# Kernel tuning notes

Hardware: AMD Instinct MI355X
Metric: run time of the kernel (lower is better)

Reference implementation:

```python
import jax, jax.numpy as jnp
import numpy as np

DIM = 1024

def setup_inputs() -> dict:
    key = jax.random.key(0)
    k1, k2, k3, k4 = jax.random.split(key, 4)
    x = jax.random.normal(k1, (4, 2048, DIM), dtype=jnp.float32)
    # nn.Linear(dim, dim).weight tensors, shape [dim, dim]
    wk = jax.random.normal(k2, (DIM, DIM), dtype=jnp.float32) * 0.02
    wq = jax.random.normal(k3, (DIM, DIM), dtype=jnp.float32) * 0.02
    wv = jax.random.normal(k4, (DIM, DIM), dtype=jnp.float32) * 0.02
    return {"x": x, "wk": wk, "wq": wq, "wv": wv}

def reference(x, wk, wq, wv):
    B, N, d = x.shape
    scale = N ** -0.5
    # stochastic value weights: softmax over dim 0 of W_v, scaled, transposed
    wv_stoch = (jax.nn.softmax(wv, axis=0) * (1.0 / d)).T
    query = x @ wq                       # [B, N, d]
    key_t = jnp.swapaxes(x @ wk, -1, -2) # [B, d, N]
    value = x @ wv_stoch                 # [B, N, d]
    scores = jnp.einsum('bnd,bdm->bnm', query, key_t) * scale  # [B, N, N]
    # softmax over dim=1 (column-wise, over queries) then subtract identity
    attn = jax.nn.softmax(scores, axis=1) - jnp.eye(N, dtype=x.dtype)
    return attn @ value
```

## Files before the change

### kernel.cpp

```cpp
#include <hip/hip_runtime.h>
#include <hip/hip_bf16.h>
#include <hip/hip_fp8.h>
#include <cstdint>
#include <cmath>

typedef __bf16 bf16_t;
typedef __bf16 bf16x8 __attribute__((ext_vector_type(8)));
typedef __bf16 bf16x4 __attribute__((ext_vector_type(4)));
typedef float floatx4 __attribute__((ext_vector_type(4)));
typedef int   intx4  __attribute__((ext_vector_type(4)));
typedef int   intx8  __attribute__((ext_vector_type(8)));

#define MB ((size_t)1 << 20)

static __device__ __forceinline__ void async_load16(const void* g, void* l) {
    __builtin_amdgcn_global_load_lds(
        (const __attribute__((address_space(1))) uint32_t*)(uintptr_t)g,
        (__attribute__((address_space(3))) uint32_t*)(uint32_t)(uintptr_t)l,
        16, 0, 0);
}

static __device__ __forceinline__ uint8_t to_fp8(float v) {
    __hip_fp8_e4m3 h(v);
    return *reinterpret_cast<uint8_t*>(&h);
}


__global__ void prep_many(const float* __restrict__ x, bf16_t* __restrict__ xb,
                          const float* __restrict__ wq, const float* __restrict__ wk,
                          bf16_t* __restrict__ wT, const float* __restrict__ wv,
                          float* __restrict__ part) {
    __shared__ float tile[32][33];
    const int bid = blockIdx.x, t = threadIdx.x;
    if (bid < 8192) {
        int i = bid * 256 + t;
        float4 v = ((const float4*)x)[i];
        bf16x4 o;
        o[0] = (bf16_t)v.x; o[1] = (bf16_t)v.y; o[2] = (bf16_t)v.z; o[3] = (bf16_t)v.w;
        ((bf16x4*)xb)[i] = o;
    } else if (bid < 10240) {
        int b2 = bid - 8192;
        const float* W = (b2 >= 1024) ? wk : wq;
        bf16_t* outp = wT + (size_t)(b2 >> 10) * 1024 * 1024;
        int b3 = b2 & 1023;
        int c0 = (b3 & 31) * 32, r0 = (b3 >> 5) * 32;
        int tx = t & 31, ty = t >> 5;
        #pragma unroll
        for (int i = 0; i < 4; i++)
            tile[ty + i * 8][tx] = W[(r0 + ty + i * 8) * 1024 + c0 + tx];
        __syncthreads();
        #pragma unroll
        for (int i = 0; i < 4; i++)
            outp[(long)(c0 + ty + i * 8) * 1024 + r0 + tx] = (bf16_t)tile[tx][ty + i * 8];
    } else {
        int b = bid - 10240;
        int d = (b & 3) * 256 + t;
        int g = b >> 2;
        float s = 0.f;
        #pragma unroll
        for (int i = 0; i < 16; i++) s += __expf(wv[(g * 16 + i) * 1024 + d]);
        part[g * 1024 + d] = s;
    }
}

__global__ void colsum_stage2(const float* __restrict__ part, float* __restrict__ cs) {
    int d = blockIdx.x * 256 + threadIdx.x;
    float s = 0.f;
    #pragma unroll 8
    for (int g = 0; g < 64; g++) s += part[g * 1024 + d];
    cs[d] = s;
}

__global__ void prep_w3(const float* __restrict__ wv, const float* __restrict__ cs,
                        bf16_t* __restrict__ w3T) {
    int idx = blockIdx.x * 256 + threadIdx.x;
    int d = idx & 1023;
    w3T[idx] = (bf16_t)(__expf(wv[idx]) / (cs[d] * 1024.0f));
}

__global__ void scale_transpose_vp(const bf16_t* __restrict__ vp,
                                   const float* __restrict__ Lpart,
                                   uint8_t* __restrict__ vpT) {
    __shared__ float tile[32][33];
    __shared__ float ls[32];
    int t = threadIdx.x;
    int tx = t & 31, ty = t >> 5;
    int e0 = blockIdx.x * 32;
    int m0 = blockIdx.y * 32;
    if (t < 32) {
        int m = m0 + t, z = m >> 11, ml = m & 2047;
        float s = 0.f;
        #pragma unroll
        for (int y = 0; y < 16; y++) s += Lpart[(z * 16 + y) * 2048 + ml];
        ls[t] = 1073741824.0f / s;
    }
    __syncthreads();
    #pragma unroll
    for (int i = 0; i < 4; i++) {
        int mr = ty + i * 8;
        tile[mr][tx] = (float)vp[(long)(m0 + mr) * 1024 + e0 + tx] * ls[mr];
    }
    __syncthreads();
    int b = m0 >> 11, ml = m0 & 2047;
    #pragma unroll
    for (int i = 0; i < 4; i++)
        vpT[((long)(b * 1024 + e0 + ty + i * 8)) * 2048 + ml + tx] = to_fp8(tile[tx][ty + i * 8]);
}

__global__ __launch_bounds__(256, 4) void gemm_qkv(
    const bf16_t* __restrict__ A, const bf16_t* __restrict__ B,
    uint8_t* __restrict__ Cq, uint8_t* __restrict__ Ck, bf16_t* __restrict__ Cv)
{
    const int K = 1024;
    __shared__ __align__(16) bf16_t ldsA[128 * 64];
    __shared__ __align__(16) bf16_t ldsB[128 * 64];
    const int t = threadIdx.x;
    const bf16_t* Ab = A + (long)blockIdx.y * 128 * K;
    const bf16_t* Bb = B + (long)blockIdx.x * 128 * K;
    const int r  = t >> 3;
    const int cg = (t & 7) ^ (r & 7);
    const bf16_t* ag0 = Ab + (long)r * K + cg * 8;
    const bf16_t* bg0 = Bb + (long)r * K + cg * 8;
    bf16_t* la = ldsA + t * 8;
    bf16_t* lb = ldsB + t * 8;
    const int lane = t & 63, wave = t >> 6;
    const int wm = (wave >> 1) * 64, wn = (wave & 1) * 64;
    const int fr = lane & 15;
    const int q4 = lane >> 4;
    const int sw = fr & 7;

    floatx4 zero = {0.f, 0.f, 0.f, 0.f};
    floatx4 acc[4][4];
    #pragma unroll
    for (int i = 0; i < 4; i++)
        #pragma unroll
        for (int j = 0; j < 4; j++) acc[i][j] = zero;

    for (int k0 = 0; k0 < K; k0 += 64) {
        __syncthreads();
        #pragma unroll
        for (int i = 0; i < 4; i++) {
            async_load16(ag0 + (long)(32 * i) * K + k0, la + 2048 * i);
            async_load16(bg0 + (long)(32 * i) * K + k0, lb + 2048 * i);
        }
        __syncthreads();
        #pragma unroll
        for (int h = 0; h < 2; h++) {
            bf16x8 af[4], bfr[4];
            #pragma unroll
            for (int i = 0; i < 4; i++) {
                int row = wm + i * 16 + fr;
                af[i] = *(const bf16x8*)(ldsA + row * 64 + (((h << 2) + q4) ^ sw) * 8);
            }
            #pragma unroll
            for (int j = 0; j < 4; j++) {
                int row = wn + j * 16 + fr;
                bfr[j] = *(const bf16x8*)(ldsB + row * 64 + (((h << 2) + q4) ^ sw) * 8);
            }
            #pragma unroll
            for (int i = 0; i < 4; i++)
                #pragma unroll
                for (int j = 0; j < 4; j++)
                    acc[i][j] = __builtin_amdgcn_mfma_f32_16x16x32_bf16(af[i], bfr[j], acc[i][j], 0, 0, 0);
        }
    }

    const int rq = (lane >> 4) * 4;
    const long rowBase = (long)blockIdx.y * 128 + wm;
    const int sel = blockIdx.x >> 3;
    const int cB = (blockIdx.x & 7) * 128 + wn;

    if (sel == 2) {
        #pragma unroll
        for (int mi = 0; mi < 4; mi++)
            #pragma unroll
            for (int rr = 0; rr < 4; rr++) {
                long row = rowBase + mi * 16 + rq + rr;
                #pragma unroll
                for (int ni = 0; ni < 4; ni++)
                    Cv[row * 1024 + cB + ni * 16 + fr] = (bf16_t)acc[mi][ni][rr];
            }
    } else {
        uint8_t* Cb = sel ? Ck : Cq;
        #pragma unroll
        for (int mi = 0; mi < 4; mi++)
            #pragma unroll
            for (int rr = 0; rr < 4; rr++) {
                long row = rowBase + mi * 16 + rq + rr;
                #pragma unroll
                for (int ni = 0; ni < 4; ni++)
                    Cb[row * 1024 + cB + ni * 16 + fr] = to_fp8(acc[mi][ni][rr]);
            }
    }
}

template <int EPI>
__global__ __launch_bounds__(256, 3) void gemm_nt_fp8(
    const uint8_t* __restrict__ A, const uint8_t* __restrict__ B, void* __restrict__ C,
    float* __restrict__ Lout, const bf16_t* __restrict__ Vp,
    int N, int K, long aBatch, long bBatch, long cBatch, float scaleExp)
{
    __shared__ __align__(16) uint8_t ldsA[128 * 128];
    __shared__ __align__(16) uint8_t ldsB[128 * 128];
    const int t = threadIdx.x;
    const int z = blockIdx.z;
    const uint8_t* Ab = A + (long)z * aBatch + (long)blockIdx.y * 128 * K;
    const uint8_t* Bb = B + (long)z * bBatch + (long)blockIdx.x * 128 * K;
    const int r  = t >> 3;
    const int cg = (t & 7) ^ (r & 7);
    const uint8_t* ag0 = Ab + (long)r * K + cg * 16;
    const uint8_t* bg0 = Bb + (long)r * K + cg * 16;
    uint8_t* la = ldsA + t * 16;
    uint8_t* lb = ldsB + t * 16;
    const int lane = t & 63, wave = t >> 6;
    const int wm = (wave >> 1) * 64, wn = (wave & 1) * 64;
    const int fr = lane & 15;
    const int q4 = lane >> 4;
    const int sw = fr & 7;

    floatx4 zero = {0.f, 0.f, 0.f, 0.f};
    floatx4 acc[4][4];
    #pragma unroll
    for (int i = 0; i < 4; i++)
        #pragma unroll
        for (int j = 0; j < 4; j++) acc[i][j] = zero;

    for (int k0 = 0; k0 < K; k0 += 128) {
        __syncthreads();
        #pragma unroll
        for (int i = 0; i < 4; i++) {
            async_load16(ag0 + (long)(32 * i) * K + k0, la + 4096 * i);
            async_load16(bg0 + (long)(32 * i) * K + k0, lb + 4096 * i);
        }
        __syncthreads();
        intx8 af[4], bfr[4];
        #pragma unroll
        for (int i = 0; i < 4; i++) {
            int row = wm + i * 16 + fr;
            intx4 lo = *(const intx4*)(ldsA + row * 128 + ((2 * q4) ^ sw) * 16);
            intx4 hi = *(const intx4*)(ldsA + row * 128 + ((2 * q4 + 1) ^ sw) * 16);
            af[i][0] = lo[0]; af[i][1] = lo[1]; af[i][2] = lo[2]; af[i][3] = lo[3];
            af[i][4] = hi[0]; af[i][5] = hi[1]; af[i][6] = hi[2]; af[i][7] = hi[3];
        }
        #pragma unroll
        for (int j = 0; j < 4; j++) {
            int row = wn + j * 16 + fr;
            intx4 lo = *(const intx4*)(ldsB + row * 128 + ((2 * q4) ^ sw) * 16);
            intx4 hi = *(const intx4*)(ldsB + row * 128 + ((2 * q4 + 1) ^ sw) * 16);
            bfr[j][0] = lo[0]; bfr[j][1] = lo[1]; bfr[j][2] = lo[2]; bfr[j][3] = lo[3];
            bfr[j][4] = hi[0]; bfr[j][5] = hi[1]; bfr[j][6] = hi[2]; bfr[j][7] = hi[3];
        }
        #pragma unroll
        for (int i = 0; i < 4; i++)
            #pragma unroll
            for (int j = 0; j < 4; j++)
                acc[i][j] = __builtin_amdgcn_mfma_scale_f32_16x16x128_f8f6f4(
                    af[i], bfr[j], acc[i][j], 0, 0,
                    0, 0x7f7f7f7f, 0, 0x7f7f7f7f);
    }

    const int rq = (lane >> 4) * 4;
    const long rowBase = (long)blockIdx.y * 128 + wm;
    const int colBase = blockIdx.x * 128 + wn;

    if constexpr (EPI == 2) {
        uint8_t* Cb = (uint8_t*)C + (long)z * cBatch;
        float csum[4] = {0.f, 0.f, 0.f, 0.f};
        #pragma unroll
        for (int mi = 0; mi < 4; mi++)
            #pragma unroll
            for (int rr = 0; rr < 4; rr++) {
                long row = rowBase + mi * 16 + rq + rr;
                #pragma unroll
                for (int ni = 0; ni < 4; ni++) {
                    float p = __expf(acc[mi][ni][rr] * scaleExp);
                    Cb[row * N + colBase + ni * 16 + fr] = to_fp8(p);
                    csum[ni] += p;
                }
            }
        float red[4];
        #pragma unroll
        for (int ni = 0; ni < 4; ni++) {
            float v = csum[ni];
            v += __shfl_xor(v, 16);
            v += __shfl_xor(v, 32);
            red[ni] = v;
        }
        __syncthreads();
        float* lf = (float*)ldsA;
        #pragma unroll
        for (int ni = 0; ni < 4; ni++)
            if (lane < 16)
                lf[(wm >> 6) * 128 + wn + ni * 16 + lane] = red[ni];
        __syncthreads();
        if (t < 128) {
            float s = lf[t] + lf[128 + t];
            Lout[(long)(z * 16 + blockIdx.y) * 2048 + blockIdx.x * 128 + t] = s;
        }
    } else {
        float* Co = (float*)C + (long)z * cBatch;
        const bf16_t* Vb = Vp + (long)z * cBatch;
        const float inv230 = 9.313225746154785e-10f;
        #pragma unroll
        for (int mi = 0; mi < 4; mi++)
            #pragma unroll
            for (int rr = 0; rr < 4; rr++) {
                long row = rowBase + mi * 16 + rq + rr;
                #pragma unroll
                for (int ni = 0; ni < 4; ni++) {
                    int col = colBase + ni * 16 + fr;
                    Co[row * N + col] = acc[mi][ni][rr] * inv230 - (float)Vb[row * N + col];
                }
            }
    }
}


extern "C" void kernel_launch(void* const* d_in, const int* in_sizes, int n_in,
                              void* d_out, int out_size, void* d_ws, size_t ws_size,
                              hipStream_t stream) {
    const float* x  = (const float*)d_in[0];
    const float* wk = (const float*)d_in[1];
    const float* wq = (const float*)d_in[2];
    const float* wv = (const float*)d_in[3];
    float* out = (float*)d_out;

    char* ws = (char*)d_ws;
    bf16_t*  P_dummy = nullptr; (void)P_dummy;
    uint8_t* P      = (uint8_t*)(ws + 0);
    bf16_t*  xb     = (bf16_t*)(ws + 0);
    bf16_t*  wqT    = (bf16_t*)(ws + 16 * MB);
    bf16_t*  w3T    = (bf16_t*)(ws + 20 * MB);
    float*   wvpart = (float*)(ws + 32 * MB);
    uint8_t* q8     = (uint8_t*)(ws + 32 * MB);
    uint8_t* vpT    = (uint8_t*)(ws + 32 * MB);
    uint8_t* k8     = (uint8_t*)(ws + 48 * MB);
    bf16_t*  vp     = (bf16_t*)(ws + 64 * MB);
    float*   cs     = (float*)(ws + 80 * MB);
    float*   Lpart  = (float*)(ws + 80 * MB + 64 * 1024);

    const float scale = 0.022097086912079608f;

    prep_many<<<10496, 256, 0, stream>>>(x, xb, wq, wk, wqT, wv, wvpart);
    colsum_stage2<<<4, 256, 0, stream>>>(wvpart, cs);
    prep_w3<<<4096, 256, 0, stream>>>(wv, cs, w3T);

    gemm_qkv<<<dim3(24, 64, 1), 256, 0, stream>>>(xb, wqT, q8, k8, vp);

    gemm_nt_fp8<2><<<dim3(16, 16, 4), 256, 0, stream>>>(q8, k8, P,
        Lpart, nullptr, 2048, 1024,
        (long)2048 * 1024, (long)2048 * 1024, (long)2048 * 2048, scale);

    scale_transpose_vp<<<dim3(32, 256), 256, 0, stream>>>(vp, Lpart, vpT);

    gemm_nt_fp8<3><<<dim3(8, 16, 4), 256, 0, stream>>>(P, vpT, out,
        nullptr, vp, 1024, 2048,
        (long)2048 * 2048, (long)1024 * 2048, (long)2048 * 1024, 0.f);
}
```

Measured before the change: 217.5 us.

## Run QKV projection in FP8 with delta-reparameterized stochastic value weights

```diff
diff --git a/kernel.cpp b/kernel.cpp
--- a/kernel.cpp
+++ b/kernel.cpp
@@ -26,22 +26,30 @@
 }
 
 
-__global__ void prep_many(const float* __restrict__ x, bf16_t* __restrict__ xb,
+__global__ void prep_many(const float* __restrict__ x, uint8_t* __restrict__ x8,
+                          float* __restrict__ Srow,
                           const float* __restrict__ wq, const float* __restrict__ wk,
-                          bf16_t* __restrict__ wT, const float* __restrict__ wv,
+                          uint8_t* __restrict__ wcat8, const float* __restrict__ wv,
                           float* __restrict__ part) {
     __shared__ float tile[32][33];
+    __shared__ float wsum[4];
     const int bid = blockIdx.x, t = threadIdx.x;
     if (bid < 8192) {
         int i = bid * 256 + t;
         float4 v = ((const float4*)x)[i];
-        bf16x4 o;
-        o[0] = (bf16_t)v.x; o[1] = (bf16_t)v.y; o[2] = (bf16_t)v.z; o[3] = (bf16_t)v.w;
-        ((bf16x4*)xb)[i] = o;
+        uint32_t pk = (uint32_t)to_fp8(v.x) | ((uint32_t)to_fp8(v.y) << 8) |
+                      ((uint32_t)to_fp8(v.z) << 16) | ((uint32_t)to_fp8(v.w) << 24);
+        ((uint32_t*)x8)[i] = pk;
+        float s = (v.x + v.y) + (v.z + v.w);
+        #pragma unroll
+        for (int d = 1; d < 64; d <<= 1) s += __shfl_xor(s, d);
+        if ((t & 63) == 0) wsum[t >> 6] = s;
+        __syncthreads();
+        if (t == 0) Srow[bid] = (wsum[0] + wsum[1]) + (wsum[2] + wsum[3]);
     } else if (bid < 10240) {
         int b2 = bid - 8192;
         const float* W = (b2 >= 1024) ? wk : wq;
-        bf16_t* outp = wT + (size_t)(b2 >> 10) * 1024 * 1024;
+        uint8_t* outp = wcat8 + (size_t)(b2 >> 10) * 1024 * 1024;
         int b3 = b2 & 1023;
         int c0 = (b3 & 31) * 32, r0 = (b3 >> 5) * 32;
         int tx = t & 31, ty = t >> 5;
@@ -51,7 +59,7 @@
         __syncthreads();
         #pragma unroll
         for (int i = 0; i < 4; i++)
-            outp[(long)(c0 + ty + i * 8) * 1024 + r0 + tx] = (bf16_t)tile[tx][ty + i * 8];
+            outp[(long)(c0 + ty + i * 8) * 1024 + r0 + tx] = to_fp8(tile[tx][ty + i * 8]);
     } else {
         int b = bid - 10240;
         int d = (b & 3) * 256 + t;
@@ -71,11 +79,12 @@
     cs[d] = s;
 }
 
-__global__ void prep_w3(const float* __restrict__ wv, const float* __restrict__ cs,
-                        bf16_t* __restrict__ w3T) {
+__global__ void prep_delta(const float* __restrict__ wv, const float* __restrict__ cs,
+                           uint8_t* __restrict__ delta8) {
     int idx = blockIdx.x * 256 + threadIdx.x;
     int d = idx & 1023;
-    w3T[idx] = (bf16_t)(__expf(wv[idx]) / (cs[d] * 1024.0f));
+    float r = __expf(wv[idx]) * 1024.0f / cs[d] - 1.0f;
+    delta8[idx] = to_fp8(r * 16.0f);
 }
 
 __global__ void scale_transpose_vp(const bf16_t* __restrict__ vp,
@@ -107,96 +116,10 @@
         vpT[((long)(b * 1024 + e0 + ty + i * 8)) * 2048 + ml + tx] = to_fp8(tile[tx][ty + i * 8]);
 }
 
-__global__ __launch_bounds__(256, 4) void gemm_qkv(
-    const bf16_t* __restrict__ A, const bf16_t* __restrict__ B,
-    uint8_t* __restrict__ Cq, uint8_t* __restrict__ Ck, bf16_t* __restrict__ Cv)
-{
-    const int K = 1024;
-    __shared__ __align__(16) bf16_t ldsA[128 * 64];
-    __shared__ __align__(16) bf16_t ldsB[128 * 64];
-    const int t = threadIdx.x;
-    const bf16_t* Ab = A + (long)blockIdx.y * 128 * K;
-    const bf16_t* Bb = B + (long)blockIdx.x * 128 * K;
-    const int r  = t >> 3;
-    const int cg = (t & 7) ^ (r & 7);
-    const bf16_t* ag0 = Ab + (long)r * K + cg * 8;
-    const bf16_t* bg0 = Bb + (long)r * K + cg * 8;
-    bf16_t* la = ldsA + t * 8;
-    bf16_t* lb = ldsB + t * 8;
-    const int lane = t & 63, wave = t >> 6;
-    const int wm = (wave >> 1) * 64, wn = (wave & 1) * 64;
-    const int fr = lane & 15;
-    const int q4 = lane >> 4;
-    const int sw = fr & 7;
-
-    floatx4 zero = {0.f, 0.f, 0.f, 0.f};
-    floatx4 acc[4][4];
-    #pragma unroll
-    for (int i = 0; i < 4; i++)
-        #pragma unroll
-        for (int j = 0; j < 4; j++) acc[i][j] = zero;
-
-    for (int k0 = 0; k0 < K; k0 += 64) {
-        __syncthreads();
-        #pragma unroll
-        for (int i = 0; i < 4; i++) {
-            async_load16(ag0 + (long)(32 * i) * K + k0, la + 2048 * i);
-            async_load16(bg0 + (long)(32 * i) * K + k0, lb + 2048 * i);
-        }
-        __syncthreads();
-        #pragma unroll
-        for (int h = 0; h < 2; h++) {
-            bf16x8 af[4], bfr[4];
-            #pragma unroll
-            for (int i = 0; i < 4; i++) {
-                int row = wm + i * 16 + fr;
-                af[i] = *(const bf16x8*)(ldsA + row * 64 + (((h << 2) + q4) ^ sw) * 8);
-            }
-            #pragma unroll
-            for (int j = 0; j < 4; j++) {
-                int row = wn + j * 16 + fr;
-                bfr[j] = *(const bf16x8*)(ldsB + row * 64 + (((h << 2) + q4) ^ sw) * 8);
-            }
-            #pragma unroll
-            for (int i = 0; i < 4; i++)
-                #pragma unroll
-                for (int j = 0; j < 4; j++)
-                    acc[i][j] = __builtin_amdgcn_mfma_f32_16x16x32_bf16(af[i], bfr[j], acc[i][j], 0, 0, 0);
-        }
-    }
-
-    const int rq = (lane >> 4) * 4;
-    const long rowBase = (long)blockIdx.y * 128 + wm;
-    const int sel = blockIdx.x >> 3;
-    const int cB = (blockIdx.x & 7) * 128 + wn;
-
-    if (sel == 2) {
-        #pragma unroll
-        for (int mi = 0; mi < 4; mi++)
-            #pragma unroll
-            for (int rr = 0; rr < 4; rr++) {
-                long row = rowBase + mi * 16 + rq + rr;
-                #pragma unroll
-                for (int ni = 0; ni < 4; ni++)
-                    Cv[row * 1024 + cB + ni * 16 + fr] = (bf16_t)acc[mi][ni][rr];
-            }
-    } else {
-        uint8_t* Cb = sel ? Ck : Cq;
-        #pragma unroll
-        for (int mi = 0; mi < 4; mi++)
-            #pragma unroll
-            for (int rr = 0; rr < 4; rr++) {
-                long row = rowBase + mi * 16 + rq + rr;
-                #pragma unroll
-                for (int ni = 0; ni < 4; ni++)
-                    Cb[row * 1024 + cB + ni * 16 + fr] = to_fp8(acc[mi][ni][rr]);
-            }
-    }
-}
-
 template <int EPI>
 __global__ __launch_bounds__(256, 3) void gemm_nt_fp8(
     const uint8_t* __restrict__ A, const uint8_t* __restrict__ B, void* __restrict__ C,
+    uint8_t* __restrict__ C1, bf16_t* __restrict__ Cv, const float* __restrict__ Srow,
     float* __restrict__ Lout, const bf16_t* __restrict__ Vp,
     int N, int K, long aBatch, long bBatch, long cBatch, float scaleExp)
 {
@@ -263,7 +186,36 @@
     const long rowBase = (long)blockIdx.y * 128 + wm;
     const int colBase = blockIdx.x * 128 + wn;
 
-    if constexpr (EPI == 2) {
+    if constexpr (EPI == 0) {
+        const int sel = blockIdx.x >> 3;
+        const int cB = (blockIdx.x & 7) * 128 + wn;
+        if (sel == 2) {
+            const float c24 = 5.9604644775390625e-08f;
+            const float c20 = 9.5367431640625e-07f;
+            #pragma unroll
+            for (int mi = 0; mi < 4; mi++)
+                #pragma unroll
+                for (int rr = 0; rr < 4; rr++) {
+                    long row = rowBase + mi * 16 + rq + rr;
+                    float sv = Srow[row] * c20;
+                    #pragma unroll
+                    for (int ni = 0; ni < 4; ni++)
+                        Cv[row * 1024 + cB + ni * 16 + fr] =
+                            (bf16_t)(acc[mi][ni][rr] * c24 + sv);
+                }
+        } else {
+            uint8_t* Cb = sel ? C1 : (uint8_t*)C;
+            #pragma unroll
+            for (int mi = 0; mi < 4; mi++)
+                #pragma unroll
+                for (int rr = 0; rr < 4; rr++) {
+                    long row = rowBase + mi * 16 + rq + rr;
+                    #pragma unroll
+                    for (int ni = 0; ni < 4; ni++)
+                        Cb[row * 1024 + cB + ni * 16 + fr] = to_fp8(acc[mi][ni][rr]);
+                }
+        }
+    } else if constexpr (EPI == 2) {
         uint8_t* Cb = (uint8_t*)C + (long)z * cBatch;
         float csum[4] = {0.f, 0.f, 0.f, 0.f};
         #pragma unroll
@@ -326,34 +278,35 @@
     float* out = (float*)d_out;
 
     char* ws = (char*)d_ws;
-    bf16_t*  P_dummy = nullptr; (void)P_dummy;
+    uint8_t* x8     = (uint8_t*)(ws + 0);
+    uint8_t* wcat8  = (uint8_t*)(ws + 8 * MB);
+    uint8_t* delta8 = wcat8 + 2u * 1024 * 1024;
     uint8_t* P      = (uint8_t*)(ws + 0);
-    bf16_t*  xb     = (bf16_t*)(ws + 0);
-    bf16_t*  wqT    = (bf16_t*)(ws + 16 * MB);
-    bf16_t*  w3T    = (bf16_t*)(ws + 20 * MB);
     float*   wvpart = (float*)(ws + 32 * MB);
     uint8_t* q8     = (uint8_t*)(ws + 32 * MB);
     uint8_t* vpT    = (uint8_t*)(ws + 32 * MB);
     uint8_t* k8     = (uint8_t*)(ws + 48 * MB);
     bf16_t*  vp     = (bf16_t*)(ws + 64 * MB);
     float*   cs     = (float*)(ws + 80 * MB);
+    float*   Srow   = (float*)(ws + 80 * MB + 16 * 1024);
     float*   Lpart  = (float*)(ws + 80 * MB + 64 * 1024);
 
     const float scale = 0.022097086912079608f;
 
-    prep_many<<<10496, 256, 0, stream>>>(x, xb, wq, wk, wqT, wv, wvpart);
+    prep_many<<<10496, 256, 0, stream>>>(x, x8, Srow, wq, wk, wcat8, wv, wvpart);
     colsum_stage2<<<4, 256, 0, stream>>>(wvpart, cs);
-    prep_w3<<<4096, 256, 0, stream>>>(wv, cs, w3T);
-
-    gemm_qkv<<<dim3(24, 64, 1), 256, 0, stream>>>(xb, wqT, q8, k8, vp);
+    prep_delta<<<4096, 256, 0, stream>>>(wv, cs, delta8);
+
+    gemm_nt_fp8<0><<<dim3(24, 64, 1), 256, 0, stream>>>(x8, wcat8, q8,
+        k8, vp, Srow, nullptr, nullptr, 1024, 1024, 0, 0, 0, 0.f);
 
     gemm_nt_fp8<2><<<dim3(16, 16, 4), 256, 0, stream>>>(q8, k8, P,
-        Lpart, nullptr, 2048, 1024,
+        nullptr, nullptr, nullptr, Lpart, nullptr, 2048, 1024,
         (long)2048 * 1024, (long)2048 * 1024, (long)2048 * 2048, scale);
 
     scale_transpose_vp<<<dim3(32, 256), 256, 0, stream>>>(vp, Lpart, vpT);
 
     gemm_nt_fp8<3><<<dim3(8, 16, 4), 256, 0, stream>>>(P, vpT, out,
-        nullptr, vp, 1024, 2048,
+        nullptr, nullptr, nullptr, nullptr, vp, 1024, 2048,
         (long)2048 * 2048, (long)1024 * 2048, (long)2048 * 1024, 0.f);
 }
```

Result: faster. 189.7 us (-12.8%).
